# Kernel optimization log

Hardware: AMD Instinct MI355X
Metric: run time of the kernel (lower is better)

## Reference

```python
import jax, jax.numpy as jnp
import numpy as np

N = 100000
E = 3200000
NFEAT, NHID, NCLASS = 256, 128, 40


def setup_inputs() -> dict:
    key = jax.random.key(0)
    ks = jax.random.split(key, 8)
    return {
        "x": jax.random.normal(ks[0], (N, NFEAT), dtype=jnp.float32),
        "edge_src": jax.random.randint(ks[1], (E,), 0, N, dtype=jnp.int32),
        "edge_dst": jax.random.randint(ks[2], (E,), 0, N, dtype=jnp.int32),
        "edge_w": jax.random.uniform(ks[3], (E,), dtype=jnp.float32),
        "W0": jax.random.normal(ks[4], (NFEAT, NHID), dtype=jnp.float32) * (2.0 / (NFEAT + NHID)) ** 0.5,
        "b0": jax.random.normal(ks[5], (1, NHID), dtype=jnp.float32) * 0.1,
        "W1": jax.random.normal(ks[6], (NHID, NCLASS), dtype=jnp.float32) * (2.0 / (NHID + NCLASS)) ** 0.5,
        "b1": jax.random.normal(ks[7], (1, NCLASS), dtype=jnp.float32) * 0.1,
    }


def _l2_normalize(h, eps=1e-12):
    # F.normalize(x, p=2, dim=1)
    nrm = jnp.sqrt(jnp.sum(h * h, axis=1, keepdims=True))
    return h / jnp.maximum(nrm, eps)


def reference(x, edge_src, edge_dst, edge_w, W0, b0, W1, b1):
    n_nodes = x.shape[0]

    def spmm(h):  # adj @ h with edge-list sparse adjacency
        return jax.ops.segment_sum(edge_w[:, None] * h[edge_src], edge_dst, num_segments=n_nodes)

    # layer 1: GraphConvolution = spmm(x @ W) + bias (dropout is identity in eval)
    h = spmm(x @ W0) + b0
    h = _l2_normalize(h)        # atg.Z1
    h = jax.nn.relu(h)          # atg.H1
    # layer 2
    z = spmm(h @ W1) + b1       # atg.Z2
    return jax.nn.log_softmax(z, axis=1)
```

## Files before the change

### kernel.cpp

```cpp
#include <hip/hip_runtime.h>
#include <math.h>

#define NN 100000
#define NE 3200000
#define NF 256
#define NH 128
#define NC 40

#define CH 8192
#define NBLK 391
#define NBUCK 782
#define HTOT (NBUCK * NBLK)
#define HS1 ((HTOT + 511) / 512)
#define NTILE 1563
#define NCP 32

typedef unsigned int uint;
typedef short short8 __attribute__((ext_vector_type(8)));
typedef float floatx4 __attribute__((ext_vector_type(4)));

__device__ __forceinline__ float bflo(uint v) { return __uint_as_float(v << 16); }
__device__ __forceinline__ float bfhi(uint v) { return __uint_as_float(v & 0xffff0000u); }
__device__ __forceinline__ unsigned short f2bf(float f) {
    const uint u = __float_as_uint(f);
    return (unsigned short)((u + 0x7fffu + ((u >> 16) & 1u)) >> 16);
}
__device__ __forceinline__ uint pack2bf(float a, float b) {
    return (uint)f2bf(a) | ((uint)f2bf(b) << 16);
}

union ABfrag { uint u[4]; short8 s; };

__global__ __launch_bounds__(256) void prep_pack_k(const float* __restrict__ W0,
                                                   const float* __restrict__ W1,
                                                   uint4* __restrict__ W0p,
                                                   uint4* __restrict__ W1p) {
    const int idx = blockIdx.x * 256 + threadIdx.x;
    if (idx < 4096) {
        const int lane  = idx & 63;
        const int ntile = (idx >> 6) & 7;
        const int kstep = idx >> 9;
        const int n  = ntile * 16 + (lane & 15);
        const int kb = kstep * 32 + (lane >> 4) * 8;
        uint w[4];
#pragma unroll
        for (int ww = 0; ww < 4; ++ww)
            w[ww] = pack2bf(W0[(size_t)(kb + 2 * ww) * NH + n],
                            W0[(size_t)(kb + 2 * ww + 1) * NH + n]);
        W0p[idx] = make_uint4(w[0], w[1], w[2], w[3]);
    } else if (idx < 4096 + 768) {
        const int i2 = idx - 4096;
        const int lane  = i2 & 63;
        const int ntile = (i2 >> 6) % 3;
        const int kstep = (i2 >> 6) / 3;
        const int n  = ntile * 16 + (lane & 15);
        const int kb = kstep * 32 + (lane >> 4) * 8;
        uint w[4];
#pragma unroll
        for (int ww = 0; ww < 4; ++ww) {
            const float lo = (n < NC) ? W1[(size_t)(kb + 2 * ww) * NC + n] : 0.0f;
            const float hi = (n < NC) ? W1[(size_t)(kb + 2 * ww + 1) * NC + n] : 0.0f;
            w[ww] = pack2bf(lo, hi);
        }
        W1p[i2] = make_uint4(w[0], w[1], w[2], w[3]);
    }
}

__global__ __launch_bounds__(256) void gemm1_mfma(const float* __restrict__ x,
                                                  const uint4* __restrict__ W0p,
                                                  unsigned short* __restrict__ xwh) {
    __shared__ __align__(16) uint4 sB[4096];
    for (int i = threadIdx.x; i < 4096; i += 256) sB[i] = W0p[i];
    __syncthreads();

    const int wave = threadIdx.x >> 6;
    const int lane = threadIdx.x & 63;
    const int quad = lane >> 4;
    const int mcol = lane & 15;

    for (int tile = blockIdx.x; tile < NTILE; tile += 512) {
        const int row  = tile * 64 + wave * 16 + mcol;
        const int rowc = min(row, NN - 1);
        const float* xr = x + (size_t)rowc * NF + quad * 8;

        floatx4 acc[8] = {};
        float4 lo = *(const float4*)(xr);
        float4 hi = *(const float4*)(xr + 4);
#pragma unroll
        for (int ks = 0; ks < 8; ++ks) {
            ABfrag a;
            a.u[0] = pack2bf(lo.x, lo.y);
            a.u[1] = pack2bf(lo.z, lo.w);
            a.u[2] = pack2bf(hi.x, hi.y);
            a.u[3] = pack2bf(hi.z, hi.w);
            if (ks < 7) {
                lo = *(const float4*)(xr + (ks + 1) * 32);
                hi = *(const float4*)(xr + (ks + 1) * 32 + 4);
            }
#pragma unroll
            for (int nt = 0; nt < 8; ++nt) {
                ABfrag b;
                const uint4 bw = sB[(ks * 8 + nt) * 64 + lane];
                b.u[0] = bw.x; b.u[1] = bw.y; b.u[2] = bw.z; b.u[3] = bw.w;
                acc[nt] = __builtin_amdgcn_mfma_f32_16x16x32_bf16(a.s, b.s, acc[nt], 0, 0, 0);
            }
        }
        const int rowbase = tile * 64 + wave * 16 + quad * 4;
#pragma unroll
        for (int nt = 0; nt < 8; ++nt) {
#pragma unroll
            for (int r = 0; r < 4; ++r) {
                const int rr = rowbase + r;
                if (rr < NN) xwh[(size_t)rr * NH + nt * 16 + mcol] = f2bf(acc[nt][r]);
            }
        }
    }
}

__global__ __launch_bounds__(256) void p1hist_k(const int* __restrict__ edst,
                                                int* __restrict__ hmat) {
    __shared__ uint h[NBUCK];
    for (int i = threadIdx.x; i < NBUCK; i += 256) h[i] = 0;
    __syncthreads();
    const int b = blockIdx.x;
    const int e0 = b * CH, e1 = min(NE, e0 + CH);
    for (int e = e0 + threadIdx.x * 4; e + 3 < e1; e += 1024) {
        const int4 d4 = *(const int4*)(edst + e);
        atomicAdd(&h[((uint)d4.x) >> 7], 1u);
        atomicAdd(&h[((uint)d4.y) >> 7], 1u);
        atomicAdd(&h[((uint)d4.z) >> 7], 1u);
        atomicAdd(&h[((uint)d4.w) >> 7], 1u);
    }
    __syncthreads();
    for (int i = threadIdx.x; i < NBUCK; i += 256)
        hmat[(size_t)i * NBLK + b] = (int)h[i];
}

__global__ __launch_bounds__(512) void hscan1_k(int* __restrict__ hmat,
                                                int* __restrict__ partials) {
    __shared__ int s[512];
    const int t = threadIdx.x;
    const int i = blockIdx.x * 512 + t;
    const int v = (i < HTOT) ? hmat[i] : 0;
    s[t] = v;
    __syncthreads();
#pragma unroll
    for (int off = 1; off < 512; off <<= 1) {
        int a = (t >= off) ? s[t - off] : 0;
        __syncthreads();
        s[t] += a;
        __syncthreads();
    }
    if (i < HTOT) hmat[i] = s[t] - v;
    if (t == 511) partials[blockIdx.x] = s[t];
}

__global__ __launch_bounds__(1024) void hscan2_k(int* __restrict__ partials, int nb) {
    __shared__ int s[1024];
    const int t = threadIdx.x;
    const int v = (t < nb) ? partials[t] : 0;
    s[t] = v;
    __syncthreads();
#pragma unroll
    for (int off = 1; off < 1024; off <<= 1) {
        int a = (t >= off) ? s[t - off] : 0;
        __syncthreads();
        s[t] += a;
        __syncthreads();
    }
    if (t < nb) partials[t] = s[t] - v;
}

__global__ __launch_bounds__(256) void p1scat_k(const int* __restrict__ esrc,
                                                const int* __restrict__ edst,
                                                const float* __restrict__ ew,
                                                const int* __restrict__ hmat,
                                                const int* __restrict__ partials,
                                                uint2* __restrict__ ep1) {
    __shared__ uint base[NBUCK];
    const int b = blockIdx.x;
    for (int i = threadIdx.x; i < NBUCK; i += 256) {
        const int g = i * NBLK + b;
        base[i] = (uint)(hmat[g] + partials[g >> 9]);
    }
    __syncthreads();
    const int e0 = b * CH, e1 = min(NE, e0 + CH);
    for (int e = e0 + threadIdx.x; e < e1; e += 256) {
        const uint d = (uint)edst[e];
        const uint pos = atomicAdd(&base[d >> 7], 1u);
        ep1[pos] = make_uint2((uint)esrc[e] | ((d & 127u) << 17), __float_as_uint(ew[e]));
    }
}

__global__ __launch_bounds__(256) void p2_k(const int* __restrict__ hmat,
                                            const int* __restrict__ partials,
                                            const uint2* __restrict__ ep1,
                                            uint2* __restrict__ ep,
                                            int* __restrict__ rp) {
    const int bk = blockIdx.x;
    const int gb = bk * NBLK;
    const int beg = hmat[gb] + partials[gb >> 9];
    int end;
    if (bk == NBUCK - 1) end = NE;
    else { const int ge = gb + NBLK; end = hmat[ge] + partials[ge >> 9]; }
    __shared__ uint cnt[128];
    __shared__ uint st[128];
    if (threadIdx.x < 128) cnt[threadIdx.x] = 0;
    __syncthreads();
    for (int j = beg + threadIdx.x; j < end; j += 256)
        atomicAdd(&cnt[(ep1[j].x >> 17) & 127u], 1u);
    __syncthreads();
    if (threadIdx.x < 128) st[threadIdx.x] = cnt[threadIdx.x];
    __syncthreads();
#pragma unroll
    for (int off = 1; off < 128; off <<= 1) {
        uint a = 0;
        if (threadIdx.x < 128 && threadIdx.x >= off) a = st[threadIdx.x - off];
        __syncthreads();
        if (threadIdx.x < 128) st[threadIdx.x] += a;
        __syncthreads();
    }
    if (threadIdx.x < 128) {
        const uint start = st[threadIdx.x] - cnt[threadIdx.x];
        const int d = bk * 128 + threadIdx.x;
        if (d < NN) rp[d] = beg + (int)start;
        cnt[threadIdx.x] = (uint)beg + start;
    }
    if (bk == 0 && threadIdx.x == 200) rp[NN] = NE;
    __syncthreads();
    for (int j = beg + threadIdx.x; j < end; j += 256) {
        const uint2 r = ep1[j];
        const uint pos = atomicAdd(&cnt[(r.x >> 17) & 127u], 1u);
        ep[pos] = r;
    }
}

__global__ __launch_bounds__(256) void spmm1n_g(const int* __restrict__ rp,
                                                const uint2* __restrict__ ep,
                                                const uint* __restrict__ xwb,
                                                const float* __restrict__ b0,
                                                uint* __restrict__ h2b) {
    const int n = blockIdx.x * 4 + (threadIdx.x >> 6);
    const int t = threadIdx.x & 63;
    const int beg = __builtin_amdgcn_readfirstlane(rp[n]);
    const int end = __builtin_amdgcn_readfirstlane(rp[n + 1]);
    float a0 = 0.f, a1 = 0.f;
    int j = beg;
    const int e8 = end - 7;
    if (j < e8) {
        uint2 e[8];
#pragma unroll
        for (int u = 0; u < 8; ++u) e[u] = ep[j + u];
        for (;;) {
            uint sx[8];
            float w[8];
#pragma unroll
            for (int u = 0; u < 8; ++u) {
                sx[u] = __builtin_amdgcn_readfirstlane(e[u].x) & 0x1FFFFu;
                w[u]  = __uint_as_float(__builtin_amdgcn_readfirstlane(e[u].y));
            }
            uint v[8];
#pragma unroll
            for (int u = 0; u < 8; ++u) v[u] = xwb[(size_t)sx[u] * 64 + t];
            j += 8;
            const bool more = (j < e8);
            if (more) {
#pragma unroll
                for (int u = 0; u < 8; ++u) e[u] = ep[j + u];
            }
#pragma unroll
            for (int u = 0; u < 8; ++u) {
                a0 = fmaf(w[u], bflo(v[u]), a0);
                a1 = fmaf(w[u], bfhi(v[u]), a1);
            }
            if (!more) break;
        }
    }
    for (; j < end; ++j) {
        const uint2 e = ep[j];
        const uint sx = __builtin_amdgcn_readfirstlane(e.x) & 0x1FFFFu;
        const float w = __uint_as_float(__builtin_amdgcn_readfirstlane(e.y));
        const uint v = xwb[(size_t)sx * 64 + t];
        a0 = fmaf(w, bflo(v), a0); a1 = fmaf(w, bfhi(v), a1);
    }
    const float2 bb = *(const float2*)(b0 + 2 * t);
    const float v0 = a0 + bb.x, v1 = a1 + bb.y;
    float s = v0 * v0 + v1 * v1;
#pragma unroll
    for (int o = 1; o < 64; o <<= 1) s += __shfl_xor(s, o, 64);
    const float scale = 1.0f / fmaxf(sqrtf(s), 1e-12f);
    h2b[(size_t)n * 64 + t] = pack2bf(fmaxf(v0 * scale, 0.0f), fmaxf(v1 * scale, 0.0f));
}

__global__ __launch_bounds__(256) void gemm2_mfma(const uint* __restrict__ h2b,
                                                  const uint4* __restrict__ W1p,
                                                  unsigned short* __restrict__ hwh) {
    __shared__ __align__(16) uint4 sB[768];
    for (int i = threadIdx.x; i < 768; i += 256) sB[i] = W1p[i];
    __syncthreads();

    const int wave = threadIdx.x >> 6;
    const int lane = threadIdx.x & 63;
    const int quad = lane >> 4;
    const int mcol = lane & 15;
    const int row  = blockIdx.x * 64 + wave * 16 + mcol;
    const int rowc = min(row, NN - 1);
    const uint* hr = h2b + (size_t)rowc * 64;

    floatx4 acc[3] = {};
#pragma unroll
    for (int ks = 0; ks < 4; ++ks) {
        ABfrag a;
        const uint4 hv = *(const uint4*)(hr + ks * 16 + quad * 4);
        a.u[0] = hv.x; a.u[1] = hv.y; a.u[2] = hv.z; a.u[3] = hv.w;
#pragma unroll
        for (int nt = 0; nt < 3; ++nt) {
            ABfrag b;
            const uint4 bw = sB[(ks * 3 + nt) * 64 + lane];
            b.u[0] = bw.x; b.u[1] = bw.y; b.u[2] = bw.z; b.u[3] = bw.w;
            acc[nt] = __builtin_amdgcn_mfma_f32_16x16x32_bf16(a.s, b.s, acc[nt], 0, 0, 0);
        }
    }
    const int rowbase = blockIdx.x * 64 + wave * 16 + quad * 4;
#pragma unroll
    for (int nt = 0; nt < 3; ++nt) {
        const int f = nt * 16 + mcol;
#pragma unroll
        for (int r = 0; r < 4; ++r) {
            const int rr = rowbase + r;
            if (rr < NN)
                hwh[(size_t)rr * (2 * NCP) + f] = (f < NC) ? f2bf(acc[nt][r]) : (unsigned short)0;
        }
    }
#pragma unroll
    for (int r = 0; r < 4; ++r) {
        const int rr = rowbase + r;
        if (rr < NN) hwh[(size_t)rr * (2 * NCP) + 48 + mcol] = (unsigned short)0;
    }
}

__global__ __launch_bounds__(256) void spmm2l_g(const int* __restrict__ rp,
                                                const uint2* __restrict__ ep,
                                                const uint* __restrict__ hwb,
                                                const float* __restrict__ b1,
                                                float2* __restrict__ out2) {
    const int n = blockIdx.x * 8 + (threadIdx.x >> 5);
    const int g = threadIdx.x & 31;
    const int beg = rp[n], end = rp[n + 1];
    float a0 = 0.f, a1 = 0.f;
    int j = beg;
    const int e8 = end - 7;
    if (j < e8) {
        uint2 e[8];
#pragma unroll
        for (int u = 0; u < 8; ++u) e[u] = ep[j + u];
        for (;;) {
            uint v[8];
#pragma unroll
            for (int u = 0; u < 8; ++u)
                v[u] = hwb[(size_t)(e[u].x & 0x1FFFFu) * NCP + g];
            float w[8];
#pragma unroll
            for (int u = 0; u < 8; ++u) w[u] = __uint_as_float(e[u].y);
            j += 8;
            const bool more = (j < e8);
            if (more) {
#pragma unroll
                for (int u = 0; u < 8; ++u) e[u] = ep[j + u];
            }
#pragma unroll
            for (int u = 0; u < 8; ++u) {
                a0 = fmaf(w[u], bflo(v[u]), a0);
                a1 = fmaf(w[u], bfhi(v[u]), a1);
            }
            if (!more) break;
        }
    }
    for (; j < end; ++j) {
        const uint2 e = ep[j];
        const uint v = hwb[(size_t)(e.x & 0x1FFFFu) * NCP + g];
        const float w = __uint_as_float(e.y);
        a0 = fmaf(w, bflo(v), a0); a1 = fmaf(w, bfhi(v), a1);
    }
    float bb0 = 0.f, bb1 = 0.f;
    if (g < 20) { const float2 bb = *(const float2*)(b1 + 2 * g); bb0 = bb.x; bb1 = bb.y; }
    a0 += bb0; a1 += bb1;
    float m = (g < 20) ? fmaxf(a0, a1) : -INFINITY;
#pragma unroll
    for (int o = 1; o < 32; o <<= 1) m = fmaxf(m, __shfl_xor(m, o, 32));
    float s = (g < 20) ? (expf(a0 - m) + expf(a1 - m)) : 0.f;
#pragma unroll
    for (int o = 1; o < 32; o <<= 1) s += __shfl_xor(s, o, 32);
    const float lse = logf(s);
    if (g < 20) out2[(size_t)n * 20 + g] = make_float2(a0 - m - lse, a1 - m - lse);
}

extern "C" void kernel_launch(void* const* d_in, const int* in_sizes, int n_in,
                              void* d_out, int out_size, void* d_ws, size_t ws_size,
                              hipStream_t stream) {
    const float* x    = (const float*)d_in[0];
    const int*   esrc = (const int*)d_in[1];
    const int*   edst = (const int*)d_in[2];
    const float* ew   = (const float*)d_in[3];
    const float* W0   = (const float*)d_in[4];
    const float* b0   = (const float*)d_in[5];
    const float* W1   = (const float*)d_in[6];
    const float* b1   = (const float*)d_in[7];
    float* out = (float*)d_out;

    size_t o = 0;
    uint*  xwb  = (uint*)d_ws + o;  o += (size_t)NN * 64;
    uint*  h2b  = (uint*)d_ws + o;  o += (size_t)NN * 64;
    uint2* ep1  = (uint2*)h2b;
    uint*  hwb  = (uint*)d_ws + o;  o += (size_t)NN * NCP;
    uint2* ep   = (uint2*)((uint*)d_ws + o); o += (size_t)NE * 2;
    int*   hmat = (int*)d_ws + o;   o += HTOT;
    int*   rp   = (int*)d_ws + o;   o += NN + 2;
    int*   partials = (int*)d_ws + o; o += 1024;
    if (o & 3) o += 4 - (o & 3);
    uint4* W0p  = (uint4*)((uint*)d_ws + o); o += 16384;
    uint4* W1p  = (uint4*)((uint*)d_ws + o); o += 3072;

    prep_pack_k<<<19, 256, 0, stream>>>(W0, W1, W0p, W1p);
    gemm1_mfma<<<512, 256, 0, stream>>>(x, W0p, (unsigned short*)xwb);

    p1hist_k<<<NBLK, 256, 0, stream>>>(edst, hmat);
    hscan1_k<<<HS1, 512, 0, stream>>>(hmat, partials);
    hscan2_k<<<1, 1024, 0, stream>>>(partials, HS1);
    p1scat_k<<<NBLK, 256, 0, stream>>>(esrc, edst, ew, hmat, partials, ep1);
    p2_k<<<NBUCK, 256, 0, stream>>>(hmat, partials, ep1, ep, rp);

    spmm1n_g<<<NN / 4, 256, 0, stream>>>(rp, ep, xwb, b0, h2b);
    gemm2_mfma<<<NTILE, 256, 0, stream>>>(h2b, W1p, (unsigned short*)hwb);
    spmm2l_g<<<NN / 8, 256, 0, stream>>>(rp, ep, hwb, b1, (float2*)out);
}
```

Baseline: 506.3 us.

## Fuse weight packing into histogram, gemm1 into bucket sort, double-buffer SpMM gathers

Weight packing now runs inside the histogram kernel, and the first GEMM runs inside the second-pass bucket-sort kernel, with blocks of each role interleaved so independent work shares a launch. The histogram pass also counts per-node degrees with global atomics. This lets the bucket pass skip its own counting sweep over ep1. Both SpMM kernels gain A/B double-buffered gathers so the loads for one group of edges overlap the FMAs of the previous group. The GEMM now reads the packed weights straight from global memory instead of staging them in LDS, and the 3.2M global atomics plus a memset add cost in exchange.

```diff
diff --git a/kernel.cpp b/kernel.cpp
--- a/kernel.cpp
+++ b/kernel.cpp
@@ -31,11 +31,12 @@
 
 union ABfrag { uint u[4]; short8 s; };
 
-__global__ __launch_bounds__(256) void prep_pack_k(const float* __restrict__ W0,
-                                                   const float* __restrict__ W1,
-                                                   uint4* __restrict__ W0p,
-                                                   uint4* __restrict__ W1p) {
-    const int idx = blockIdx.x * 256 + threadIdx.x;
+__device__ __forceinline__ void prep_body(int pidx,
+                                          const float* __restrict__ W0,
+                                          const float* __restrict__ W1,
+                                          uint4* __restrict__ W0p,
+                                          uint4* __restrict__ W1p) {
+    const int idx = pidx * 256 + threadIdx.x;
     if (idx < 4096) {
         const int lane  = idx & 63;
         const int ntile = (idx >> 6) & 7;
@@ -66,63 +67,20 @@
     }
 }
 
-__global__ __launch_bounds__(256) void gemm1_mfma(const float* __restrict__ x,
-                                                  const uint4* __restrict__ W0p,
-                                                  unsigned short* __restrict__ xwh) {
-    __shared__ __align__(16) uint4 sB[4096];
-    for (int i = threadIdx.x; i < 4096; i += 256) sB[i] = W0p[i];
-    __syncthreads();
-
-    const int wave = threadIdx.x >> 6;
-    const int lane = threadIdx.x & 63;
-    const int quad = lane >> 4;
-    const int mcol = lane & 15;
-
-    for (int tile = blockIdx.x; tile < NTILE; tile += 512) {
-        const int row  = tile * 64 + wave * 16 + mcol;
-        const int rowc = min(row, NN - 1);
-        const float* xr = x + (size_t)rowc * NF + quad * 8;
-
-        floatx4 acc[8] = {};
-        float4 lo = *(const float4*)(xr);
-        float4 hi = *(const float4*)(xr + 4);
-#pragma unroll
-        for (int ks = 0; ks < 8; ++ks) {
-            ABfrag a;
-            a.u[0] = pack2bf(lo.x, lo.y);
-            a.u[1] = pack2bf(lo.z, lo.w);
-            a.u[2] = pack2bf(hi.x, hi.y);
-            a.u[3] = pack2bf(hi.z, hi.w);
-            if (ks < 7) {
-                lo = *(const float4*)(xr + (ks + 1) * 32);
-                hi = *(const float4*)(xr + (ks + 1) * 32 + 4);
-            }
-#pragma unroll
-            for (int nt = 0; nt < 8; ++nt) {
-                ABfrag b;
-                const uint4 bw = sB[(ks * 8 + nt) * 64 + lane];
-                b.u[0] = bw.x; b.u[1] = bw.y; b.u[2] = bw.z; b.u[3] = bw.w;
-                acc[nt] = __builtin_amdgcn_mfma_f32_16x16x32_bf16(a.s, b.s, acc[nt], 0, 0, 0);
-            }
-        }
-        const int rowbase = tile * 64 + wave * 16 + quad * 4;
-#pragma unroll
-        for (int nt = 0; nt < 8; ++nt) {
-#pragma unroll
-            for (int r = 0; r < 4; ++r) {
-                const int rr = rowbase + r;
-                if (rr < NN) xwh[(size_t)rr * NH + nt * 16 + mcol] = f2bf(acc[nt][r]);
-            }
-        }
-    }
-}
-
-__global__ __launch_bounds__(256) void p1hist_k(const int* __restrict__ edst,
-                                                int* __restrict__ hmat) {
+__global__ __launch_bounds__(256) void k1_hist_prep(const int* __restrict__ edst,
+                                                    int* __restrict__ hmat,
+                                                    int* __restrict__ ndeg,
+                                                    const float* __restrict__ W0,
+                                                    const float* __restrict__ W1,
+                                                    uint4* __restrict__ W0p,
+                                                    uint4* __restrict__ W1p) {
     __shared__ uint h[NBUCK];
+    const int bid = blockIdx.x;
+    if (bid < 38 && (bid & 1)) { prep_body(bid >> 1, W0, W1, W0p, W1p); return; }
+    const int b = (bid < 38) ? (bid >> 1) : (bid - 19);
+
     for (int i = threadIdx.x; i < NBUCK; i += 256) h[i] = 0;
     __syncthreads();
-    const int b = blockIdx.x;
     const int e0 = b * CH, e1 = min(NE, e0 + CH);
     for (int e = e0 + threadIdx.x * 4; e + 3 < e1; e += 1024) {
         const int4 d4 = *(const int4*)(edst + e);
@@ -130,6 +88,10 @@
         atomicAdd(&h[((uint)d4.y) >> 7], 1u);
         atomicAdd(&h[((uint)d4.z) >> 7], 1u);
         atomicAdd(&h[((uint)d4.w) >> 7], 1u);
+        atomicAdd(&ndeg[d4.x], 1);
+        atomicAdd(&ndeg[d4.y], 1);
+        atomicAdd(&ndeg[d4.z], 1);
+        atomicAdd(&ndeg[d4.w], 1);
     }
     __syncthreads();
     for (int i = threadIdx.x; i < NBUCK; i += 256)
@@ -192,48 +154,121 @@
     }
 }
 
-__global__ __launch_bounds__(256) void p2_k(const int* __restrict__ hmat,
-                                            const int* __restrict__ partials,
-                                            const uint2* __restrict__ ep1,
-                                            uint2* __restrict__ ep,
-                                            int* __restrict__ rp) {
-    const int bk = blockIdx.x;
+__device__ __forceinline__ void p2_body(int bk,
+                                        const int* __restrict__ hmat,
+                                        const int* __restrict__ partials,
+                                        const int* __restrict__ ndeg,
+                                        const uint2* __restrict__ ep1,
+                                        uint2* __restrict__ ep,
+                                        int* __restrict__ rp) {
     const int gb = bk * NBLK;
     const int beg = hmat[gb] + partials[gb >> 9];
-    int end;
-    if (bk == NBUCK - 1) end = NE;
-    else { const int ge = gb + NBLK; end = hmat[ge] + partials[ge >> 9]; }
     __shared__ uint cnt[128];
     __shared__ uint st[128];
-    if (threadIdx.x < 128) cnt[threadIdx.x] = 0;
-    __syncthreads();
-    for (int j = beg + threadIdx.x; j < end; j += 256)
-        atomicAdd(&cnt[(ep1[j].x >> 17) & 127u], 1u);
-    __syncthreads();
-    if (threadIdx.x < 128) st[threadIdx.x] = cnt[threadIdx.x];
+    __shared__ int send;
+    const int t = threadIdx.x;
+    uint c = 0;
+    if (t < 128) {
+        const int d = bk * 128 + t;
+        c = (d < NN) ? (uint)ndeg[d] : 0u;
+        st[t] = c;
+    }
     __syncthreads();
 #pragma unroll
     for (int off = 1; off < 128; off <<= 1) {
         uint a = 0;
-        if (threadIdx.x < 128 && threadIdx.x >= off) a = st[threadIdx.x - off];
-        __syncthreads();
-        if (threadIdx.x < 128) st[threadIdx.x] += a;
-        __syncthreads();
-    }
-    if (threadIdx.x < 128) {
-        const uint start = st[threadIdx.x] - cnt[threadIdx.x];
-        const int d = bk * 128 + threadIdx.x;
+        if (t < 128 && t >= off) a = st[t - off];
+        __syncthreads();
+        if (t < 128) st[t] += a;
+        __syncthreads();
+    }
+    if (t < 128) {
+        const uint start = st[t] - c;
+        const int d = bk * 128 + t;
         if (d < NN) rp[d] = beg + (int)start;
-        cnt[threadIdx.x] = (uint)beg + start;
-    }
-    if (bk == 0 && threadIdx.x == 200) rp[NN] = NE;
-    __syncthreads();
-    for (int j = beg + threadIdx.x; j < end; j += 256) {
+        cnt[t] = (uint)beg + start;
+        if (t == 127) send = beg + (int)st[127];
+    }
+    if (bk == 0 && t == 200) rp[NN] = NE;
+    __syncthreads();
+    const int end = send;
+    for (int j = beg + t; j < end; j += 256) {
         const uint2 r = ep1[j];
         const uint pos = atomicAdd(&cnt[(r.x >> 17) & 127u], 1u);
         ep[pos] = r;
     }
 }
+
+__device__ __forceinline__ void gemm1_body(int bstart,
+                                           const float* __restrict__ x,
+                                           const uint4* __restrict__ W0p,
+                                           unsigned short* __restrict__ xwh) {
+    const int wave = threadIdx.x >> 6;
+    const int lane = threadIdx.x & 63;
+    const int quad = lane >> 4;
+    const int mcol = lane & 15;
+
+    for (int tile = bstart; tile < NTILE; tile += 512) {
+        const int row  = tile * 64 + wave * 16 + mcol;
+        const int rowc = min(row, NN - 1);
+        const float* xr = x + (size_t)rowc * NF + quad * 8;
+
+        floatx4 acc[8] = {};
+        float4 lo = *(const float4*)(xr);
+        float4 hi = *(const float4*)(xr + 4);
+#pragma unroll
+        for (int ks = 0; ks < 8; ++ks) {
+            ABfrag a;
+            a.u[0] = pack2bf(lo.x, lo.y);
+            a.u[1] = pack2bf(lo.z, lo.w);
+            a.u[2] = pack2bf(hi.x, hi.y);
+            a.u[3] = pack2bf(hi.z, hi.w);
+            if (ks < 7) {
+                lo = *(const float4*)(xr + (ks + 1) * 32);
+                hi = *(const float4*)(xr + (ks + 1) * 32 + 4);
+            }
+#pragma unroll
+            for (int nt = 0; nt < 8; ++nt) {
+                ABfrag b;
+                const uint4 bw = W0p[(ks * 8 + nt) * 64 + lane];
+                b.u[0] = bw.x; b.u[1] = bw.y; b.u[2] = bw.z; b.u[3] = bw.w;
+                acc[nt] = __builtin_amdgcn_mfma_f32_16x16x32_bf16(a.s, b.s, acc[nt], 0, 0, 0);
+            }
+        }
+        const int rowbase = tile * 64 + wave * 16 + quad * 4;
+#pragma unroll
+        for (int nt = 0; nt < 8; ++nt) {
+#pragma unroll
+            for (int r = 0; r < 4; ++r) {
+                const int rr = rowbase + r;
+                if (rr < NN) xwh[(size_t)rr * NH + nt * 16 + mcol] = f2bf(acc[nt][r]);
+            }
+        }
+    }
+}
+
+__global__ __launch_bounds__(256) void k2_p2_gemm1(const int* __restrict__ hmat,
+                                                   const int* __restrict__ partials,
+                                                   const int* __restrict__ ndeg,
+                                                   const uint2* __restrict__ ep1,
+                                                   uint2* __restrict__ ep,
+                                                   int* __restrict__ rp,
+                                                   const float* __restrict__ x,
+                                                   const uint4* __restrict__ W0p,
+                                                   unsigned short* __restrict__ xwh) {
+    const int bid = blockIdx.x;
+    if (bid < 1024 && (bid & 1)) { gemm1_body(bid >> 1, x, W0p, xwh); return; }
+    const int bk = (bid < 1024) ? (bid >> 1) : (bid - 512);
+    p2_body(bk, hmat, partials, ndeg, ep1, ep, rp);
+}
+
+#define LD8(m, base) _Pragma("unroll") for (int u = 0; u < 8; ++u) m[u] = ep[(base) + u];
+#define DEC8(s, w, m) _Pragma("unroll") for (int u = 0; u < 8; ++u) { \
+        s[u] = ((uint)__builtin_amdgcn_readfirstlane(m[u].x)) & 0x1FFFFu; \
+        w[u] = __uint_as_float((uint)__builtin_amdgcn_readfirstlane(m[u].y)); }
+#define GAT8(v, s) _Pragma("unroll") for (int u = 0; u < 8; ++u) v[u] = xwb[(size_t)s[u] * 64 + t];
+#define ACC8(v, w) _Pragma("unroll") for (int u = 0; u < 8; ++u) { \
+        a0 = fmaf(w[u], bflo(v[u]), a0); a1 = fmaf(w[u], bfhi(v[u]), a1); }
 
 __global__ __launch_bounds__(256) void spmm1n_g(const int* __restrict__ rp,
                                                 const uint2* __restrict__ ep,
@@ -246,40 +281,38 @@
     const int end = __builtin_amdgcn_readfirstlane(rp[n + 1]);
     float a0 = 0.f, a1 = 0.f;
     int j = beg;
-    const int e8 = end - 7;
-    if (j < e8) {
-        uint2 e[8];
-#pragma unroll
-        for (int u = 0; u < 8; ++u) e[u] = ep[j + u];
-        for (;;) {
-            uint sx[8];
-            float w[8];
-#pragma unroll
-            for (int u = 0; u < 8; ++u) {
-                sx[u] = __builtin_amdgcn_readfirstlane(e[u].x) & 0x1FFFFu;
-                w[u]  = __uint_as_float(__builtin_amdgcn_readfirstlane(e[u].y));
+    const int endf = beg + ((end - beg) & ~7);
+    if (j < endf) {
+        uint sA[8]; float wA[8]; uint vA[8];
+        { uint2 m[8]; LD8(m, j); DEC8(sA, wA, m); GAT8(vA, sA); }
+        int jn = j + 8;
+        if (jn < endf) {
+            uint sB[8]; float wB[8]; uint vB[8];
+            { uint2 m[8]; LD8(m, jn); DEC8(sB, wB, m); GAT8(vB, sB); }
+            jn += 8;
+            for (;;) {
+                if (jn < endf) {
+                    uint2 m[8]; LD8(m, jn);
+                    ACC8(vA, wA);
+                    DEC8(sA, wA, m); GAT8(vA, sA);
+                    jn += 8;
+                } else { ACC8(vA, wA); ACC8(vB, wB); break; }
+                if (jn < endf) {
+                    uint2 m[8]; LD8(m, jn);
+                    ACC8(vB, wB);
+                    DEC8(sB, wB, m); GAT8(vB, sB);
+                    jn += 8;
+                } else { ACC8(vB, wB); ACC8(vA, wA); break; }
             }
-            uint v[8];
-#pragma unroll
-            for (int u = 0; u < 8; ++u) v[u] = xwb[(size_t)sx[u] * 64 + t];
-            j += 8;
-            const bool more = (j < e8);
-            if (more) {
-#pragma unroll
-                for (int u = 0; u < 8; ++u) e[u] = ep[j + u];
-            }
-#pragma unroll
-            for (int u = 0; u < 8; ++u) {
-                a0 = fmaf(w[u], bflo(v[u]), a0);
-                a1 = fmaf(w[u], bfhi(v[u]), a1);
-            }
-            if (!more) break;
-        }
+        } else {
+            ACC8(vA, wA);
+        }
+        j = endf;
     }
     for (; j < end; ++j) {
         const uint2 e = ep[j];
-        const uint sx = __builtin_amdgcn_readfirstlane(e.x) & 0x1FFFFu;
-        const float w = __uint_as_float(__builtin_amdgcn_readfirstlane(e.y));
+        const uint sx = ((uint)__builtin_amdgcn_readfirstlane(e.x)) & 0x1FFFFu;
+        const float w = __uint_as_float((uint)__builtin_amdgcn_readfirstlane(e.y));
         const uint v = xwb[(size_t)sx * 64 + t];
         a0 = fmaf(w, bflo(v), a0); a1 = fmaf(w, bfhi(v), a1);
     }
@@ -338,6 +371,10 @@
         if (rr < NN) hwh[(size_t)rr * (2 * NCP) + 48 + mcol] = (unsigned short)0;
     }
 }
+
+#define DEC8L(s, w, m) _Pragma("unroll") for (int u = 0; u < 8; ++u) { \
+        s[u] = m[u].x & 0x1FFFFu; w[u] = __uint_as_float(m[u].y); }
+#define GAT8L(v, s) _Pragma("unroll") for (int u = 0; u < 8; ++u) v[u] = hwb[(size_t)s[u] * NCP + g];
 
 __global__ __launch_bounds__(256) void spmm2l_g(const int* __restrict__ rp,
                                                 const uint2* __restrict__ ep,
@@ -349,32 +386,33 @@
     const int beg = rp[n], end = rp[n + 1];
     float a0 = 0.f, a1 = 0.f;
     int j = beg;
-    const int e8 = end - 7;
-    if (j < e8) {
-        uint2 e[8];
-#pragma unroll
-        for (int u = 0; u < 8; ++u) e[u] = ep[j + u];
-        for (;;) {
-            uint v[8];
-#pragma unroll
-            for (int u = 0; u < 8; ++u)
-                v[u] = hwb[(size_t)(e[u].x & 0x1FFFFu) * NCP + g];
-            float w[8];
-#pragma unroll
-            for (int u = 0; u < 8; ++u) w[u] = __uint_as_float(e[u].y);
-            j += 8;
-            const bool more = (j < e8);
-            if (more) {
-#pragma unroll
-                for (int u = 0; u < 8; ++u) e[u] = ep[j + u];
+    const int endf = beg + ((end - beg) & ~7);
+    if (j < endf) {
+        uint sA[8]; float wA[8]; uint vA[8];
+        { uint2 m[8]; LD8(m, j); DEC8L(sA, wA, m); GAT8L(vA, sA); }
+        int jn = j + 8;
+        if (jn < endf) {
+            uint sB[8]; float wB[8]; uint vB[8];
+            { uint2 m[8]; LD8(m, jn); DEC8L(sB, wB, m); GAT8L(vB, sB); }
+            jn += 8;
+            for (;;) {
+                if (jn < endf) {
+                    uint2 m[8]; LD8(m, jn);
+                    ACC8(vA, wA);
+                    DEC8L(sA, wA, m); GAT8L(vA, sA);
+                    jn += 8;
+                } else { ACC8(vA, wA); ACC8(vB, wB); break; }
+                if (jn < endf) {
+                    uint2 m[8]; LD8(m, jn);
+                    ACC8(vB, wB);
+                    DEC8L(sB, wB, m); GAT8L(vB, sB);
+                    jn += 8;
+                } else { ACC8(vB, wB); ACC8(vA, wA); break; }
             }
-#pragma unroll
-            for (int u = 0; u < 8; ++u) {
-                a0 = fmaf(w[u], bflo(v[u]), a0);
-                a1 = fmaf(w[u], bfhi(v[u]), a1);
-            }
-            if (!more) break;
-        }
+        } else {
+            ACC8(vA, wA);
+        }
+        j = endf;
     }
     for (; j < end; ++j) {
         const uint2 e = ep[j];
@@ -417,18 +455,21 @@
     int*   hmat = (int*)d_ws + o;   o += HTOT;
     int*   rp   = (int*)d_ws + o;   o += NN + 2;
     int*   partials = (int*)d_ws + o; o += 1024;
+    int*   ndeg = (int*)d_ws + o;   o += NN;
     if (o & 3) o += 4 - (o & 3);
     uint4* W0p  = (uint4*)((uint*)d_ws + o); o += 16384;
     uint4* W1p  = (uint4*)((uint*)d_ws + o); o += 3072;
 
-    prep_pack_k<<<19, 256, 0, stream>>>(W0, W1, W0p, W1p);
-    gemm1_mfma<<<512, 256, 0, stream>>>(x, W0p, (unsigned short*)xwb);
-
-    p1hist_k<<<NBLK, 256, 0, stream>>>(edst, hmat);
+    hipMemsetAsync(ndeg, 0, (size_t)NN * sizeof(int), stream);
+
+    k1_hist_prep<<<410, 256, 0, stream>>>(edst, hmat, ndeg, W0, W1, W0p, W1p);
+
     hscan1_k<<<HS1, 512, 0, stream>>>(hmat, partials);
     hscan2_k<<<1, 1024, 0, stream>>>(partials, HS1);
     p1scat_k<<<NBLK, 256, 0, stream>>>(esrc, edst, ew, hmat, partials, ep1);
-    p2_k<<<NBUCK, 256, 0, stream>>>(hmat, partials, ep1, ep, rp);
+
+    k2_p2_gemm1<<<1294, 256, 0, stream>>>(hmat, partials, ndeg, ep1, ep, rp,
+                                          x, W0p, (unsigned short*)xwb);
 
     spmm1n_g<<<NN / 4, 256, 0, stream>>>(rp, ep, xwb, b0, h2b);
     gemm2_mfma<<<NTILE, 256, 0, stream>>>(h2b, W1p, (unsigned short*)hwb);
```

New measurement: 670.7 us. 32.5% more time.
